# Kernel optimization log

Hardware: AMD Instinct MI355X
Metric: run time of the kernel (lower is better)

Reference implementation:

```python
import jax, jax.numpy as jnp
import numpy as np

# Dims: B=batch, T=seq, D=input=256=F*F, H=hidden=256=F*F, F=16 factor, R=16 TT rank, 4 gates (I,F,G,O)
F, R, NG = 16, 16, 4


def setup_inputs():
    key = jax.random.key(0)
    ks = jax.random.split(key, 11)
    s = 0.1  # core init scale keeps gate pre-activations O(1)
    inp = {
        "x": jax.random.normal(ks[0], (64, 1024, 256), jnp.float32),
        # TT cores for the 4 input-to-hidden gates (boundary ranks squeezed)
        "ih_g0": s * jax.random.normal(ks[1], (NG, F, R), jnp.float32),
        "ih_g1": s * jax.random.normal(ks[2], (NG, R, F, R), jnp.float32),
        "ih_g2": s * jax.random.normal(ks[3], (NG, R, F, R), jnp.float32),
        "ih_g3": s * jax.random.normal(ks[4], (NG, R, F), jnp.float32),
        "ih_bias": jnp.zeros((NG, F * F), jnp.float32),
        # TT cores for the 4 hidden-to-hidden gates
        "hh_g0": s * jax.random.normal(ks[5], (NG, F, R), jnp.float32),
        "hh_g1": s * jax.random.normal(ks[6], (NG, R, F, R), jnp.float32),
        "hh_g2": s * jax.random.normal(ks[7], (NG, R, F, R), jnp.float32),
        "hh_g3": s * jax.random.normal(ks[8], (NG, R, F), jnp.float32),
        "hh_bias": jnp.zeros((NG, F * F), jnp.float32),
    }
    return inp


def tt_linear(x2, g0, g1, g2, g3, bias):
    # x2: [N, F*F] -> contract TT cores per gate g -> [N, NG, F*F]
    n = x2.shape[0]
    x3 = x2.reshape(n, F, F)
    t = jnp.einsum('bmn,gmr->bgnr', x3, g0)      # contract first input factor
    t = jnp.einsum('bgnr,grns->bgs', t, g1)      # contract second input factor
    t = jnp.einsum('bgs,gsot->bgot', t, g2)      # emit first output factor
    y = jnp.einsum('bgot,gtp->bgop', t, g3)      # emit second output factor
    return y.reshape(n, NG, F * F) + bias        # bias: [NG, F*F]


def reference(x, ih_g0, ih_g1, ih_g2, ih_g3, ih_bias,
              hh_g0, hh_g1, hh_g2, hh_g3, hh_bias):
    B, T, D = x.shape
    H = F * F
    # Precompute input-to-hidden gate contributions for all timesteps at once
    ih_all = tt_linear(x.reshape(B * T, D), ih_g0, ih_g1, ih_g2, ih_g3, ih_bias)
    ih_all = ih_all.reshape(B, T, NG, H).transpose(1, 0, 2, 3)  # [T,B,4,H]

    def step(carry, ih_t):
        h, c = carry
        gates = ih_t + tt_linear(h, hh_g0, hh_g1, hh_g2, hh_g3, hh_bias)
        i = jax.nn.sigmoid(gates[:, 0])
        f = jax.nn.sigmoid(gates[:, 1])
        g = jnp.tanh(gates[:, 2])
        o = jax.nn.sigmoid(gates[:, 3])
        c = f * c + i * g
        h = o * jnp.tanh(c)
        return (h, c), h

    h0 = jnp.zeros((B, H), x.dtype)
    c0 = jnp.zeros((B, H), x.dtype)
    (h, c), ys = jax.lax.scan(step, (h0, c0), ih_all)
    output = ys.transpose(1, 0, 2)  # [B,T,H]
    return output, (h, c)
```

## Files before the change

kernel.cpp:

```cpp
#include <hip/hip_runtime.h>


#define WS_A1I 0
#define WS_A1H 16384
#define WS_C2I 32768
#define WS_C2H 49152
#define WS_BIAS 65536
#define WS_T2 66560

typedef float v2f __attribute__((ext_vector_type(2)));

__device__ __forceinline__ v2f pk_fma(v2f a, v2f b, v2f c) {
    v2f d;
    asm("v_pk_fma_f32 %0, %1, %2, %3" : "=v"(d) : "v"(a), "v"(b), "v"(c));
    return d;
}

__device__ __forceinline__ void bar_lds() {
    asm volatile("s_waitcnt lgkmcnt(0)\n\ts_barrier" ::: "memory");
}

template <int CTRL>
__device__ __forceinline__ float dpp_add(float v) {
    int s = __builtin_amdgcn_update_dpp(0, __float_as_int(v), CTRL, 0xF, 0xF, true);
    return v + __int_as_float(s);
}
template <int CTRL>
__device__ __forceinline__ float dpp_bcast(float v) {
    int s = __builtin_amdgcn_update_dpp(0, __float_as_int(v), CTRL, 0xF, 0xF, true);
    return __int_as_float(s);
}

__global__ void k_compose(const float* __restrict__ g0i, const float* __restrict__ g1i,
                          const float* __restrict__ g2i, const float* __restrict__ g3i,
                          const float* __restrict__ bi,
                          const float* __restrict__ g0h, const float* __restrict__ g1h,
                          const float* __restrict__ g2h, const float* __restrict__ g3h,
                          const float* __restrict__ bh,
                          float* __restrict__ ws) {
    int id = blockIdx.x * 256 + threadIdx.x;
    if (id < 16384) {
        int g = id >> 12, s = (id >> 8) & 15, mn = id & 255;
        int m = mn >> 4, n = mn & 15;
        float aI = 0.f, aH = 0.f;
        for (int r = 0; r < 16; ++r) {
            aI += g0i[(g * 16 + m) * 16 + r] * g1i[((g * 16 + r) * 16 + n) * 16 + s];
            aH += g0h[(g * 16 + m) * 16 + r] * g1h[((g * 16 + r) * 16 + n) * 16 + s];
        }
        ws[WS_A1I + (g * 16 + s) * 256 + mn] = aI;
        ws[WS_A1H + (g * 16 + s) * 256 + mn] = aH;
    } else if (id < 32768) {
        int id2 = id - 16384;
        int g = id2 >> 12, s = (id2 >> 8) & 15, j = id2 & 255;
        int o = j >> 4, p = j & 15;
        float aI = 0.f, aH = 0.f;
        for (int t = 0; t < 16; ++t) {
            aI += g2i[((g * 16 + s) * 16 + o) * 16 + t] * g3i[(g * 16 + t) * 16 + p];
            aH += g2h[((g * 16 + s) * 16 + o) * 16 + t] * g3h[(g * 16 + t) * 16 + p];
        }
        ws[WS_C2I + (g * 16 + s) * 256 + j] = aI;
        ws[WS_C2H + (g * 16 + s) * 256 + j] = aH;
    } else if (id < 33792) {
        int id2 = id - 32768;
        ws[WS_BIAS + id2] = bi[id2] + bh[id2];
    }
}

__global__ __launch_bounds__(256, 2) void k_t2ih(const float* __restrict__ x,
                                                 const float* __restrict__ ws,
                                                 float* __restrict__ T2) {
    __shared__ __align__(16) float Xs[64 * 128];
    __shared__ __align__(16) float As[64 * 128];
    const int tid = threadIdx.x;
    const long r0 = (long)blockIdx.x * 64;
    const int ro = tid & 15;
    const int q  = tid >> 4;

    const float4* X4g = (const float4*)x;
    const float4* A4  = (const float4*)(ws + WS_A1I);
    float4* Xs4 = (float4*)Xs;
    float4* As4 = (float4*)As;

    v2f acc2[4][4];
#pragma unroll
    for (int i = 0; i < 4; ++i)
#pragma unroll
        for (int j = 0; j < 4; ++j) acc2[i][j] = (v2f){0.f, 0.f};

    for (int half = 0; half < 2; ++half) {
        __syncthreads();
#pragma unroll
        for (int k = 0; k < 8; ++k) {
            int idx = k * 256 + tid;
            int row = idx >> 5, c = idx & 31;
            int sw = (row << 5) | (c ^ ((row >> 2) & 15));
            Xs4[sw] = X4g[(r0 + row) * 64 + half * 32 + c];
            As4[sw] = A4[row * 64 + half * 32 + c];
        }
        __syncthreads();

#pragma unroll 4
        for (int mn4 = 0; mn4 < 32; ++mn4) {
            float4 a[4], xv[4];
#pragma unroll
            for (int j = 0; j < 4; ++j) {
                int row = ro * 4 + j;
                a[j] = As4[(row << 5) | (mn4 ^ ro)];
            }
#pragma unroll
            for (int i = 0; i < 4; ++i) {
                int row = q * 4 + i;
                xv[i] = Xs4[(row << 5) | (mn4 ^ q)];
            }
#pragma unroll
            for (int i = 0; i < 4; ++i)
#pragma unroll
                for (int j = 0; j < 4; ++j) {
                    acc2[i][j] = pk_fma((v2f){xv[i].x, xv[i].y},
                                        (v2f){a[j].x, a[j].y}, acc2[i][j]);
                    acc2[i][j] = pk_fma((v2f){xv[i].z, xv[i].w},
                                        (v2f){a[j].z, a[j].w}, acc2[i][j]);
                }
        }
    }
#pragma unroll
    for (int i = 0; i < 4; ++i)
#pragma unroll
        for (int j = 0; j < 4; ++j)
            T2[(r0 + q * 4 + i) * 64 + ro * 4 + j] = acc2[i][j].x + acc2[i][j].y;
}

__global__ __launch_bounds__(512, 2) void k_lstm(const float* __restrict__ ws,
                                                 const float* __restrict__ T2,
                                                 float* __restrict__ out) {
    __shared__ __align__(16) float hS[256];
    __shared__ __align__(16) float t2hS[64];
    __shared__ __align__(16) float t2iS[2][64];

    const int tid  = threadIdx.x;
    const int w    = tid >> 6;
    const int lane = tid & 63;
    const int b    = blockIdx.x;

    const int uab = 4 * w + (lane >> 4);
    const int sub = lane & 15;
    v2f a1p0[8], a1p1[8];
    {
        const float4* A1h4 = (const float4*)(ws + WS_A1H);
#pragma unroll
        for (int kk = 0; kk < 4; ++kk) {
            float4 v0 = A1h4[uab * 64 + sub * 4 + kk];
            float4 v1 = A1h4[(uab + 32) * 64 + sub * 4 + kk];
            a1p0[2 * kk + 0] = (v2f){v0.x, v0.y};
            a1p0[2 * kk + 1] = (v2f){v0.z, v0.w};
            a1p1[2 * kk + 0] = (v2f){v1.x, v1.y};
            a1p1[2 * kk + 1] = (v2f){v1.z, v1.w};
        }
    }

    const int jj = lane >> 2;
    const int g  = lane & 3;
    const int j0 = 16 * w + jj;
    const int j1 = j0 + 128;
    v2f c2hp0[8], c2ip0[8], c2hp1[8], c2ip1[8];
#pragma unroll
    for (int qq = 0; qq < 4; ++qq) {
#pragma unroll
        for (int hh = 0; hh < 2; ++hh) {
            int s0 = 16 * g + 4 * qq + 2 * hh;
            c2hp0[2 * qq + hh] = (v2f){ws[WS_C2H + (s0 + 0) * 256 + j0],
                                       ws[WS_C2H + (s0 + 1) * 256 + j0]};
            c2ip0[2 * qq + hh] = (v2f){ws[WS_C2I + (s0 + 0) * 256 + j0],
                                       ws[WS_C2I + (s0 + 1) * 256 + j0]};
            c2hp1[2 * qq + hh] = (v2f){ws[WS_C2H + (s0 + 0) * 256 + j1],
                                       ws[WS_C2H + (s0 + 1) * 256 + j1]};
            c2ip1[2 * qq + hh] = (v2f){ws[WS_C2I + (s0 + 0) * 256 + j1],
                                       ws[WS_C2I + (s0 + 1) * 256 + j1]};
        }
    }
    float bias0 = ws[WS_BIAS + g * 256 + j0];
    float bias1 = ws[WS_BIAS + g * 256 + j1];
    const float am = (g == 2) ? 2.0f : 1.0f;
    const float as = 1.442695040888963f * am;

#pragma unroll
    for (int i = 0; i < 8; ++i)
        asm volatile("" : "+v"(a1p0[i]), "+v"(a1p1[i]), "+v"(c2hp0[i]),
                         "+v"(c2ip0[i]), "+v"(c2hp1[i]), "+v"(c2ip1[i]));

    const int hw0 = ((jj >> 2) << 6) + 4 * w + (jj & 3);
    const int hw1 = hw0 + 32;

    float c0 = 0.f, c1 = 0.f, h0l = 0.f, h1l = 0.f;
    if (tid < 256) hS[tid] = 0.f;
    const float* T2b = T2 + (long)b * 1024 * 64;
    const float4* T2b4 = (const float4*)T2b;
    float4 preA = make_float4(0.f, 0.f, 0.f, 0.f);
    float4 preB = make_float4(0.f, 0.f, 0.f, 0.f);
    if (tid < 16) {
        ((float4*)t2iS[0])[tid] = T2b4[tid];
        preA = T2b4[16 + tid];
    }
    bar_lds();

    float* outB = out + (long)b * 1024 * 256;
    const float4* hS4 = (const float4*)hS;
    const float4* th4 = (const float4*)t2hS;

    auto body = [&](int t, float4& preW, float4& preL) {
        v2f sA0 = (v2f){0.f, 0.f}, sB0 = (v2f){0.f, 0.f};
        v2f sA1 = (v2f){0.f, 0.f}, sB1 = (v2f){0.f, 0.f};
#pragma unroll
        for (int kk = 0; kk < 4; ++kk) {
            float4 hv = hS4[kk * 16 + sub];
            v2f hxy = (v2f){hv.x, hv.y}, hzw = (v2f){hv.z, hv.w};
            sA0 = pk_fma(hxy, a1p0[2 * kk + 0], sA0);
            sB0 = pk_fma(hzw, a1p0[2 * kk + 1], sB0);
            sA1 = pk_fma(hxy, a1p1[2 * kk + 0], sA1);
            sB1 = pk_fma(hzw, a1p1[2 * kk + 1], sB1);
        }
        float tv0 = (sA0.x + sA0.y) + (sB0.x + sB0.y);
        float tv1 = (sA1.x + sA1.y) + (sB1.x + sB1.y);
        if ((tid < 16) && (t + 1 < 1024))
            ((float4*)t2iS[(t + 1) & 1])[tid] = preW;
        if ((tid < 16) && (t + 2 < 1024))
            preL = T2b4[(t + 2) * 16 + tid];
        tv0 = dpp_add<0x111>(tv0);  tv1 = dpp_add<0x111>(tv1);
        tv0 = dpp_add<0x112>(tv0);  tv1 = dpp_add<0x112>(tv1);
        tv0 = dpp_add<0x114>(tv0);  tv1 = dpp_add<0x114>(tv1);
        tv0 = dpp_add<0x118>(tv0);  tv1 = dpp_add<0x118>(tv1);
        if (sub == 15) {
            t2hS[uab]      = tv0;
            t2hS[uab + 32] = tv1;
        }

        bar_lds();

        const float4* ti4 = (const float4*)t2iS[t & 1];
        v2f aH0 = (v2f){bias0, 0.f}, aL0 = (v2f){0.f, 0.f};
        v2f aH1 = (v2f){bias1, 0.f}, aL1 = (v2f){0.f, 0.f};
#pragma unroll
        for (int qq = 0; qq < 4; ++qq) {
            float4 th = th4[g * 4 + qq];
            float4 ti = ti4[g * 4 + qq];
            v2f txy = (v2f){th.x, th.y}, tzw = (v2f){th.z, th.w};
            v2f ixy = (v2f){ti.x, ti.y}, izw = (v2f){ti.z, ti.w};
            aH0 = pk_fma(txy, c2hp0[2 * qq + 0], aH0);
            aL0 = pk_fma(tzw, c2hp0[2 * qq + 1], aL0);
            aH1 = pk_fma(txy, c2hp1[2 * qq + 0], aH1);
            aL1 = pk_fma(tzw, c2hp1[2 * qq + 1], aL1);
            aH0 = pk_fma(ixy, c2ip0[2 * qq + 0], aH0);
            aL0 = pk_fma(izw, c2ip0[2 * qq + 1], aL0);
            aH1 = pk_fma(ixy, c2ip1[2 * qq + 0], aH1);
            aL1 = pk_fma(izw, c2ip1[2 * qq + 1], aL1);
        }
        float acc0 = (aH0.x + aH0.y) + (aL0.x + aL0.y);
        float acc1 = (aH1.x + aH1.y) + (aL1.x + aL1.y);
        float e0   = __builtin_amdgcn_exp2f(as * acc0);
        float e1   = __builtin_amdgcn_exp2f(as * acc1);
        float act0 = 1.0f - am * __builtin_amdgcn_rcpf(1.0f + e0);
        float act1 = 1.0f - am * __builtin_amdgcn_rcpf(1.0f + e1);
        float gi0 = dpp_bcast<0x00>(act0), gi1 = dpp_bcast<0x00>(act1);
        float gf0 = dpp_bcast<0x55>(act0), gf1 = dpp_bcast<0x55>(act1);
        float gg0 = dpp_bcast<0xAA>(act0), gg1 = dpp_bcast<0xAA>(act1);
        float go0 = dpp_bcast<0xFF>(act0), go1 = dpp_bcast<0xFF>(act1);
        c0 = gf0 * c0 + gi0 * gg0;
        c1 = gf1 * c1 + gi1 * gg1;
        float ex0 = __builtin_amdgcn_exp2f(2.885390081777926f * c0);
        float ex1 = __builtin_amdgcn_exp2f(2.885390081777926f * c1);
        float th0 = 1.0f - 2.0f * __builtin_amdgcn_rcpf(1.0f + ex0);
        float th1 = 1.0f - 2.0f * __builtin_amdgcn_rcpf(1.0f + ex1);
        float h0 = go0 * th0;
        float h1 = go1 * th1;
        h0l = h0; h1l = h1;
        if (g == 0) {
            hS[hw0] = h0;
            hS[hw1] = h1;
            outB[t * 256 + j0] = h0;
            outB[t * 256 + j1] = h1;
        }

        bar_lds();
    };

    for (int t = 0; t < 1024; t += 2) {
        body(t, preA, preB);
        body(t + 1, preB, preA);
    }

    if (g == 0) {
        out[16777216 + b * 256 + j0] = h0l;
        out[16777216 + b * 256 + j1] = h1l;
        out[16777216 + 16384 + b * 256 + j0] = c0;
        out[16777216 + 16384 + b * 256 + j1] = c1;
    }
}

extern "C" void kernel_launch(void* const* d_in, const int* in_sizes, int n_in,
                              void* d_out, int out_size, void* d_ws, size_t ws_size,
                              hipStream_t stream) {
    const float* x     = (const float*)d_in[0];
    const float* ih_g0 = (const float*)d_in[1];
    const float* ih_g1 = (const float*)d_in[2];
    const float* ih_g2 = (const float*)d_in[3];
    const float* ih_g3 = (const float*)d_in[4];
    const float* ih_b  = (const float*)d_in[5];
    const float* hh_g0 = (const float*)d_in[6];
    const float* hh_g1 = (const float*)d_in[7];
    const float* hh_g2 = (const float*)d_in[8];
    const float* hh_g3 = (const float*)d_in[9];
    const float* hh_b  = (const float*)d_in[10];
    float* out = (float*)d_out;
    float* ws  = (float*)d_ws;

    k_compose<<<132, 256, 0, stream>>>(ih_g0, ih_g1, ih_g2, ih_g3, ih_b,
                                       hh_g0, hh_g1, hh_g2, hh_g3, hh_b, ws);
    k_t2ih<<<1024, 256, 0, stream>>>(x, ws, ws + WS_T2);
    k_lstm<<<64, 512, 0, stream>>>(ws, ws + WS_T2, out);
}
```

Measured before the change: 845.0 us.

## Retile input projection GEMM to 256-row blocks with register prefetch double-buffering

The input-to-hidden projection kernel now processes 256 rows per block with an 8x8 per-thread register tile instead of 64 rows with 4x4. The full 64x256 A matrix stays resident in LDS, and the X tiles stream through in eight K-chunks using register prefetch into double-buffered LDS. Output stores become float4. This aims to raise arithmetic intensity and overlap global loads with FMAs, at the cost of heavy register pressure (128 accumulator floats plus operands), occupancy of one block per CU, and only 256 blocks in the grid.

```diff
diff --git a/kernel.cpp b/kernel.cpp
--- a/kernel.cpp
+++ b/kernel.cpp
@@ -66,68 +66,94 @@
     }
 }
 
-__global__ __launch_bounds__(256, 2) void k_t2ih(const float* __restrict__ x,
+__global__ __launch_bounds__(256, 1) void k_t2ih(const float* __restrict__ x,
                                                  const float* __restrict__ ws,
                                                  float* __restrict__ T2) {
-    __shared__ __align__(16) float Xs[64 * 128];
-    __shared__ __align__(16) float As[64 * 128];
+    __shared__ __align__(16) float4 As4[64 * 64];
+    __shared__ __align__(16) float4 Xs4[2][256 * 8];
     const int tid = threadIdx.x;
-    const long r0 = (long)blockIdx.x * 64;
-    const int ro = tid & 15;
-    const int q  = tid >> 4;
+    const long r0 = (long)blockIdx.x * 256;
+    const int rg = tid >> 3;
+    const int ug = tid & 7;
 
     const float4* X4g = (const float4*)x;
     const float4* A4  = (const float4*)(ws + WS_A1I);
-    float4* Xs4 = (float4*)Xs;
-    float4* As4 = (float4*)As;
-
-    v2f acc2[4][4];
-#pragma unroll
-    for (int i = 0; i < 4; ++i)
-#pragma unroll
-        for (int j = 0; j < 4; ++j) acc2[i][j] = (v2f){0.f, 0.f};
-
-    for (int half = 0; half < 2; ++half) {
-        __syncthreads();
-#pragma unroll
-        for (int k = 0; k < 8; ++k) {
-            int idx = k * 256 + tid;
-            int row = idx >> 5, c = idx & 31;
-            int sw = (row << 5) | (c ^ ((row >> 2) & 15));
-            Xs4[sw] = X4g[(r0 + row) * 64 + half * 32 + c];
-            As4[sw] = A4[row * 64 + half * 32 + c];
-        }
-        __syncthreads();
-
-#pragma unroll 4
-        for (int mn4 = 0; mn4 < 32; ++mn4) {
-            float4 a[4], xv[4];
-#pragma unroll
-            for (int j = 0; j < 4; ++j) {
-                int row = ro * 4 + j;
-                a[j] = As4[(row << 5) | (mn4 ^ ro)];
+
+#pragma unroll
+    for (int it = 0; it < 16; ++it) {
+        int idx = it * 256 + tid;
+        int u = idx >> 6, k4 = idx & 63;
+        As4[u * 64 + (k4 & ~7) + ((k4 + (u >> 3)) & 7)] = A4[idx];
+    }
+#pragma unroll
+    for (int it = 0; it < 8; ++it) {
+        int idx = it * 256 + tid;
+        int row = idx >> 3, c4 = idx & 7;
+        Xs4[0][row * 8 + ((c4 + (row >> 3)) & 7)] = X4g[(r0 + row) * 64 + c4];
+    }
+    __syncthreads();
+
+    v2f acc[8][8];
+#pragma unroll
+    for (int i = 0; i < 8; ++i)
+#pragma unroll
+        for (int uu = 0; uu < 8; ++uu) acc[i][uu] = (v2f){0.f, 0.f};
+
+    float4 xr[8];
+    for (int kc = 0; kc < 8; ++kc) {
+        if (kc + 1 < 8) {
+#pragma unroll
+            for (int it = 0; it < 8; ++it) {
+                int idx = it * 256 + tid;
+                int row = idx >> 3, c4 = idx & 7;
+                xr[it] = X4g[(r0 + row) * 64 + (kc + 1) * 8 + c4];
             }
-#pragma unroll
-            for (int i = 0; i < 4; ++i) {
-                int row = q * 4 + i;
-                xv[i] = Xs4[(row << 5) | (mn4 ^ q)];
+        }
+        const float4* Xb = Xs4[kc & 1];
+#pragma unroll
+        for (int k4 = 0; k4 < 8; ++k4) {
+            float4 xv[8], av[8];
+#pragma unroll
+            for (int i = 0; i < 8; ++i)
+                xv[i] = Xb[(rg * 8 + i) * 8 + ((k4 + rg) & 7)];
+#pragma unroll
+            for (int uu = 0; uu < 8; ++uu)
+                av[uu] = As4[(ug * 8 + uu) * 64 + kc * 8 + ((k4 + ug) & 7)];
+#pragma unroll
+            for (int i = 0; i < 8; ++i)
+#pragma unroll
+                for (int uu = 0; uu < 8; ++uu) {
+                    acc[i][uu] = pk_fma((v2f){xv[i].x, xv[i].y},
+                                        (v2f){av[uu].x, av[uu].y}, acc[i][uu]);
+                    acc[i][uu] = pk_fma((v2f){xv[i].z, xv[i].w},
+                                        (v2f){av[uu].z, av[uu].w}, acc[i][uu]);
+                }
+        }
+        if (kc + 1 < 8) {
+#pragma unroll
+            for (int it = 0; it < 8; ++it) {
+                int idx = it * 256 + tid;
+                int row = idx >> 3, c4 = idx & 7;
+                Xs4[(kc + 1) & 1][row * 8 + ((c4 + (row >> 3)) & 7)] = xr[it];
             }
-#pragma unroll
-            for (int i = 0; i < 4; ++i)
-#pragma unroll
-                for (int j = 0; j < 4; ++j) {
-                    acc2[i][j] = pk_fma((v2f){xv[i].x, xv[i].y},
-                                        (v2f){a[j].x, a[j].y}, acc2[i][j]);
-                    acc2[i][j] = pk_fma((v2f){xv[i].z, xv[i].w},
-                                        (v2f){a[j].z, a[j].w}, acc2[i][j]);
-                }
-        }
-    }
-#pragma unroll
-    for (int i = 0; i < 4; ++i)
-#pragma unroll
-        for (int j = 0; j < 4; ++j)
-            T2[(r0 + q * 4 + i) * 64 + ro * 4 + j] = acc2[i][j].x + acc2[i][j].y;
+            __syncthreads();
+        }
+    }
+
+    float4* T24 = (float4*)T2;
+#pragma unroll
+    for (int i = 0; i < 8; ++i) {
+        long row = r0 + rg * 8 + i;
+#pragma unroll
+        for (int s = 0; s < 2; ++s) {
+            float4 o;
+            o.x = acc[i][4 * s + 0].x + acc[i][4 * s + 0].y;
+            o.y = acc[i][4 * s + 1].x + acc[i][4 * s + 1].y;
+            o.z = acc[i][4 * s + 2].x + acc[i][4 * s + 2].y;
+            o.w = acc[i][4 * s + 3].x + acc[i][4 * s + 3].y;
+            T24[row * 16 + ug * 2 + s] = o;
+        }
+    }
 }
 
 __global__ __launch_bounds__(512, 2) void k_lstm(const float* __restrict__ ws,
@@ -315,6 +341,6 @@
 
     k_compose<<<132, 256, 0, stream>>>(ih_g0, ih_g1, ih_g2, ih_g3, ih_b,
                                        hh_g0, hh_g1, hh_g2, hh_g3, hh_b, ws);
-    k_t2ih<<<1024, 256, 0, stream>>>(x, ws, ws + WS_T2);
+    k_t2ih<<<256, 256, 0, stream>>>(x, ws, ws + WS_T2);
     k_lstm<<<64, 512, 0, stream>>>(ws, ws + WS_T2, out);
 }
```

Measured after the change: 879.3 us. +4.1%, slower.
